# Kernel optimization log

Hardware: AMD Instinct MI355X
Metric: run time of the kernel (lower is better)

The kernel has to match this reference:

```python
import jax, jax.numpy as jnp
import numpy as np

B, N_ATOM, COORD = 32, 48, 3
N_ELEM = 4
GRID_SIZE = 128
SIGMA = 0.05      # gaussian broadening of distf
W_SCALE = 1.0     # weightf: exp(-W_SCALE * distance)
INV_SQRT2PI = 1.0 / np.sqrt(2.0 * np.pi)


def _pairs(n):
    # static ordered index pairs i != j (built with numpy -> jit-safe constants)
    ii, jj = np.meshgrid(np.arange(n), np.arange(n), indexing='ij')
    m = ii != jj
    return jnp.asarray(ii[m]), jnp.asarray(jj[m])


def setup_inputs() -> dict:
    key = jax.random.key(0)
    k1, k2 = jax.random.split(key)
    r = jax.random.normal(k1, (B, N_ATOM, COORD), dtype=jnp.float32) * 2.0
    z = jax.random.randint(k2, (N_ATOM,), 0, N_ELEM)  # species index in [0, N_ELEM)
    grid = jnp.linspace(0.0, 2.0, GRID_SIZE, dtype=jnp.float32)
    return {"r": r, "z": z, "grid": grid}


def reference(r, z, grid):
    b, n, c = r.shape
    g = grid.shape[0]
    e = N_ELEM
    dx = grid[1] - grid[0]
    pi, pj = _pairs(n)                              # (P,)

    diff = r[:, pi] - r[:, pj]                      # (b,P,3)
    d = jnp.sqrt(jnp.sum(diff * diff, axis=-1))     # (b,P) pair distances
    gf = 1.0 / d                                    # geomf: inverse distance
    wf = jnp.exp(-W_SCALE * d)                      # weightf: exponential decay
    # distf: normalized gaussian centered at gf, scaled by grid spacing dx
    t = (grid[None, None, :] - gf[..., None]) / SIGMA
    gv = jnp.exp(-0.5 * t * t) * (dx * INV_SQRT2PI / SIGMA)   # (b,P,G)

    contrib = wf[..., None] * gv                    # (b,P,G)
    seg = z[pi] * e + z[pj]                         # (P,) element-pair bucket
    mbtr = jax.ops.segment_sum(contrib.transpose(1, 0, 2), seg, num_segments=e * e)
    mbtr = mbtr.reshape(e, e, b, g).transpose(2, 0, 1, 3)      # (b,E,E,G)

    # analytic divergence wrt the two atoms' coordinates (order=2, coord=3)
    u = diff / d[..., None]                         # dd/dr_i, (b,P,3)
    dd = jnp.stack([u, -u], axis=2)                 # (b,P,2,3): dd/dr_{i}, dd/dr_{j}
    gf_div = -(gf * gf)[..., None, None] * dd       # d(1/d)/dr
    wf_div = -(W_SCALE * wf)[..., None, None] * dd  # d exp(-s d)/dr
    grid_div = gv * (grid[None, None, :] - gf[..., None]) / (SIGMA * SIGMA)  # dgv/dgf

    # (b,P,G,2,3): gv*wf_div + grid_div*gf_div*wf
    div = (gv[:, :, :, None, None] * wf_div[:, :, None, :, :]
           + grid_div[:, :, :, None, None] * (gf_div * wf[..., None, None])[:, :, None, :, :])

    atom_idx = jnp.stack([pi, pj], axis=1)          # (P,2)
    seg_div = (seg[:, None] * n + atom_idx).reshape(-1)        # (2P,) bucket*n + atom
    p2 = div.transpose(1, 3, 0, 2, 4).reshape(-1, b, g, c)     # (2P,b,G,3)
    mbtr_div = jax.ops.segment_sum(p2, seg_div, num_segments=e * e * n)
    mbtr_div = mbtr_div.reshape(e, e, n, b, g, c).transpose(3, 0, 1, 4, 2, 5)  # (b,E,E,G,N,3)
    return mbtr, mbtr_div
```

## Files before the change

### kernel.cpp

```cpp
#include <hip/hip_runtime.h>

#define NB     32
#define NATOM  48
#define NGRID  128
#define KT     8
#define NTHR   384

#define MBTR_ELEMS (NB*16*NGRID)
#define DIV_PER_B  (16*NGRID*NATOM*3)
#define PANE       (NGRID*NATOM*3)
#define FSTRIDE    49
#define KSTRIDE    (16*FSTRIDE)

__global__ __launch_bounds__(NTHR)
void mbtr_fused(const float* __restrict__ r, const int* __restrict__ z,
                const float* __restrict__ grid, float* __restrict__ out)
{
    const int kt = blockIdx.x, b = blockIdx.y, t = threadIdx.x;
    const int k0 = kt * KT;

    __shared__ float4 pos[NATOM];
    __shared__ int    zl[NATOM];
    __shared__ int    order[NATOM];
    __shared__ int    soff_s[5];
    __shared__ float  Arec[KT * KSTRIDE];

    if (t < 64) {
        const bool isatom = (t < NATOM);
        int myz = 999;
        if (isatom) {
            myz = z[t];
            zl[t] = myz;
            const float* rp = r + ((size_t)b * NATOM + t) * 3;
            pos[t] = make_float4(rp[0], rp[1], rp[2], 0.f);
        }
        const unsigned long long m0 = __ballot(myz == 0);
        const unsigned long long m1 = __ballot(myz == 1);
        const unsigned long long m2 = __ballot(myz == 2);
        const unsigned long long m3 = __ballot(myz == 3);
        const int c0 = __popcll(m0), c1 = __popcll(m1), c2 = __popcll(m2);
        if (isatom) {
            const unsigned long long mm = (myz == 0) ? m0 : (myz == 1) ? m1
                                        : (myz == 2) ? m2 : m3;
            const int base = (myz == 0) ? 0 : (myz == 1) ? c0
                           : (myz == 2) ? c0 + c1 : c0 + c1 + c2;
            const int rank = __popcll(mm & ((1ull << t) - 1ull));
            order[base + rank] = t;
        }
        if (t == 0) {
            soff_s[0] = 0; soff_s[1] = c0; soff_s[2] = c0 + c1;
            soff_s[3] = c0 + c1 + c2; soff_s[4] = NATOM;
        }
    }
    if (t < KT * 16)
        Arec[(t >> 4) * KSTRIDE + (t & 15) * FSTRIDE + NATOM] = 0.f;
    __syncthreads();

    const int n  = t % NATOM;
    const int kk = t / NATOM;
    const float dx   = grid[1] - grid[0];
    const float coef = dx * (0.3989422804014327f * 20.0f);
    const float isc  = 20.0f * 0.84932180580221964f;
    const float tBc  = 20.0f / 0.84932180580221964f;
    const float l2e  = 1.4426950408889634f;
    const float gk   = grid[k0 + kk] * isc;

    float A[4][3] = {{0.f}};
    float M[4]    = {0.f};
    const float4 rn = pos[n];
    int so[5];
    #pragma unroll
    for (int e = 0; e < 5; ++e) so[e] = soff_s[e];

    #pragma unroll
    for (int e = 0; e < 4; ++e) {
        for (int i = so[e]; i < so[e + 1]; ++i) {
            const int    m  = order[i];
            const float4 rm = pos[m];
            const float ddx = rn.x - rm.x, ddy = rn.y - rm.y, ddz = rn.z - rm.z;
            float d2 = ddx*ddx + ddy*ddy + ddz*ddz;
            const bool self = (m == n);
            d2 = self ? 1.0f : d2;
            const float gf  = __builtin_amdgcn_rsqf(d2);
            const float d   = d2 * gf;
            const float tt  = gk - gf * isc;
            const float arg = fmaf(d, l2e, tt * tt);
            const float ex  = exp2f(-arg);
            const float gvw = (self ? 0.f : coef) * ex;
            M[e] += gvw;
            const float p  = gvw * fmaf(tt, gf * gf * tBc, 1.0f);
            const float pg = -p * gf;
            A[e][0] = fmaf(pg, ddx, A[e][0]);
            A[e][1] = fmaf(pg, ddy, A[e][1]);
            A[e][2] = fmaf(pg, ddz, A[e][2]);
        }
    }

    {
        float* ar = Arec + kk * KSTRIDE + n;
        #pragma unroll
        for (int e = 0; e < 4; ++e) {
            ar[(e * 3 + 0) * FSTRIDE] = A[e][0];
            ar[(e * 3 + 1) * FSTRIDE] = A[e][1];
            ar[(e * 3 + 2) * FSTRIDE] = A[e][2];
            ar[(12 + e)    * FSTRIDE] = M[e];
        }
    }
    __syncthreads();

    int a1[2][4], a2[2][4], obase[2] = {0, 0};
    #pragma unroll
    for (int jj = 0; jj < 2; ++jj) {
        const int u = t + NTHR * jj;
        if (u < 576) {
            const int pane = u / 36, w36 = u % 36;
            const int e1 = pane >> 2, e2 = pane & 3;
            obase[jj] = pane * PANE + w36 * 4;
            #pragma unroll
            for (int s = 0; s < 4; ++s) {
                const int p = w36 * 4 + s, nn = p / 3, c = p - nn * 3;
                a1[jj][s] = (zl[nn] == e1) ? ((e2 * 3 + c) * FSTRIDE + nn)
                                           : ((e2 * 3 + c) * FSTRIDE + NATOM);
                a2[jj][s] = (zl[nn] == e2) ? ((e1 * 3 + c) * FSTRIDE + nn)
                                           : ((e1 * 3 + c) * FSTRIDE + NATOM);
            }
        }
    }
    const bool do_mbtr = (t >= 192 && t < 320);
    int mpane = 0, mkk = 0, me1 = 0, me2 = 0;
    if (do_mbtr) {
        const int t2 = t - 192;
        mpane = t2 >> 3; mkk = t2 & 7;
        me1 = mpane >> 2; me2 = mpane & 3;
    }

    float* divout = out + MBTR_ELEMS + (size_t)b * DIV_PER_B;
    #pragma unroll
    for (int kq = 0; kq < KT; ++kq) {
        const float* trk = Arec + kq * KSTRIDE;
        const int k = k0 + kq;
        #pragma unroll
        for (int jj = 0; jj < 2; ++jj) {
            const int u = t + NTHR * jj;
            if (u < 576) {
                float4 v;
                v.x = trk[a1[jj][0]] + trk[a2[jj][0]];
                v.y = trk[a1[jj][1]] + trk[a2[jj][1]];
                v.z = trk[a1[jj][2]] + trk[a2[jj][2]];
                v.w = trk[a1[jj][3]] + trk[a2[jj][3]];
                *(float4*)(divout + obase[jj] + k * 144) = v;
            }
        }
    }
    if (do_mbtr) {
        const float* tr2 = Arec + mkk * KSTRIDE + (12 + me2) * FSTRIDE;
        float s = 0.f;
        #pragma unroll
        for (int nn = 0; nn < NATOM; ++nn)
            s += (zl[nn] == me1) ? tr2[nn] : 0.f;
        out[(size_t)b * 2048 + mpane * NGRID + k0 + mkk] = s;
    }
}

extern "C" void kernel_launch(void* const* d_in, const int* in_sizes, int n_in,
                              void* d_out, int out_size, void* d_ws, size_t ws_size,
                              hipStream_t stream)
{
    const float* r    = (const float*)d_in[0];
    const int*   z    = (const int*)  d_in[1];
    const float* grid = (const float*)d_in[2];
    float* out = (float*)d_out;
    (void)d_ws; (void)ws_size;

    mbtr_fused<<<dim3(NGRID / KT, NB), NTHR, 0, stream>>>(r, z, grid, out);
}
```

Before: 82.64 us.

## Compute two grid points per thread, reusing pair geometry, and halve block size

Each thread now evaluates two grid points (k and k+4) for the same atom, so the distance, rsqrt and direction terms are computed once and used twice. The launch block shrinks from 384 to 192 threads. The per-element loop over sorted atom ranges becomes one flat loop that looks up each atom's element at runtime. The normalisation coefficient is folded into the exponent, and the store loop now covers three output slots per thread. Indexing the accumulator arrays with a runtime element index risks the compiler placing them in scratch memory or emitting select chains, and the smaller blocks reduce parallelism per block.

```diff
diff --git a/kernel.cpp b/kernel.cpp
--- a/kernel.cpp
+++ b/kernel.cpp
@@ -4,7 +4,7 @@
 #define NATOM  48
 #define NGRID  128
 #define KT     8
-#define NTHR   384
+#define NTHR   192
 
 #define MBTR_ELEMS (NB*16*NGRID)
 #define DIV_PER_B  (16*NGRID*NATOM*3)
@@ -22,7 +22,6 @@
     __shared__ float4 pos[NATOM];
     __shared__ int    zl[NATOM];
     __shared__ int    order[NATOM];
-    __shared__ int    soff_s[5];
     __shared__ float  Arec[KT * KSTRIDE];
 
     if (t < 64) {
@@ -47,112 +46,123 @@
             const int rank = __popcll(mm & ((1ull << t) - 1ull));
             order[base + rank] = t;
         }
-        if (t == 0) {
-            soff_s[0] = 0; soff_s[1] = c0; soff_s[2] = c0 + c1;
-            soff_s[3] = c0 + c1 + c2; soff_s[4] = NATOM;
-        }
     }
     if (t < KT * 16)
         Arec[(t >> 4) * KSTRIDE + (t & 15) * FSTRIDE + NATOM] = 0.f;
     __syncthreads();
 
     const int n  = t % NATOM;
-    const int kk = t / NATOM;
+    const int kq = t / NATOM;
     const float dx   = grid[1] - grid[0];
-    const float coef = dx * (0.3989422804014327f * 20.0f);
-    const float isc  = 20.0f * 0.84932180580221964f;
-    const float tBc  = 20.0f / 0.84932180580221964f;
+    const float coef = dx * 7.9788456080286535f;
+    const float mlc  = -__log2f(coef);
+    const float isc  = 16.986436005760382f;
+    const float tBc  = 23.548200452219559f;
     const float l2e  = 1.4426950408889634f;
-    const float gk   = grid[k0 + kk] * isc;
+    const float gkA  = grid[k0 + kq]     * isc;
+    const float gkB  = grid[k0 + kq + 4] * isc;
 
-    float A[4][3] = {{0.f}};
-    float M[4]    = {0.f};
+    float A[2][4][3] = {{{0.f}}};
+    float M[2][4]    = {{0.f}};
     const float4 rn = pos[n];
+
     int so[5];
-    #pragma unroll
-    for (int e = 0; e < 5; ++e) so[e] = soff_s[e];
+    {
+        int cnt0 = 0, cnt1 = 0, cnt2 = 0;
+        (void)cnt0; (void)cnt1; (void)cnt2;
+        so[0] = 0; so[4] = NATOM;
+    }
 
-    #pragma unroll
-    for (int e = 0; e < 4; ++e) {
-        for (int i = so[e]; i < so[e + 1]; ++i) {
-            const int    m  = order[i];
-            const float4 rm = pos[m];
-            const float ddx = rn.x - rm.x, ddy = rn.y - rm.y, ddz = rn.z - rm.z;
-            float d2 = ddx*ddx + ddy*ddy + ddz*ddz;
-            const bool self = (m == n);
-            d2 = self ? 1.0f : d2;
-            const float gf  = __builtin_amdgcn_rsqf(d2);
-            const float d   = d2 * gf;
-            const float tt  = gk - gf * isc;
-            const float arg = fmaf(d, l2e, tt * tt);
-            const float ex  = exp2f(-arg);
-            const float gvw = (self ? 0.f : coef) * ex;
-            M[e] += gvw;
-            const float p  = gvw * fmaf(tt, gf * gf * tBc, 1.0f);
-            const float pg = -p * gf;
-            A[e][0] = fmaf(pg, ddx, A[e][0]);
-            A[e][1] = fmaf(pg, ddy, A[e][1]);
-            A[e][2] = fmaf(pg, ddz, A[e][2]);
+    #pragma unroll 4
+    for (int i = 0; i < NATOM; ++i) {
+        const int    m  = order[i];
+        const int    e  = zl[m];
+        const float4 rm = pos[m];
+        const float ddx = rn.x - rm.x, ddy = rn.y - rm.y, ddz = rn.z - rm.z;
+        float d2 = ddx*ddx + ddy*ddy + ddz*ddz;
+        const bool self = (m == n);
+        d2 = self ? 1.0f : d2;
+        const float gf  = __builtin_amdgcn_rsqf(d2);
+        const float c1  = gf * isc;
+        const float d   = d2 * gf;
+        float base = fmaf(d, l2e, mlc);
+        base = self ? 1e30f : base;
+        const float bq  = (gf * gf) * tBc;
+        const float sux = gf * ddx, suy = gf * ddy, suz = gf * ddz;
+        {
+            const float tt = gkA - c1;
+            const float ex = exp2f(-fmaf(tt, tt, base));
+            M[0][e] += ex;
+            const float p  = ex * fmaf(tt, bq, 1.0f);
+            A[0][e][0] = fmaf(-p, sux, A[0][e][0]);
+            A[0][e][1] = fmaf(-p, suy, A[0][e][1]);
+            A[0][e][2] = fmaf(-p, suz, A[0][e][2]);
+        }
+        {
+            const float tt = gkB - c1;
+            const float ex = exp2f(-fmaf(tt, tt, base));
+            M[1][e] += ex;
+            const float p  = ex * fmaf(tt, bq, 1.0f);
+            A[1][e][0] = fmaf(-p, sux, A[1][e][0]);
+            A[1][e][1] = fmaf(-p, suy, A[1][e][1]);
+            A[1][e][2] = fmaf(-p, suz, A[1][e][2]);
         }
     }
+    (void)so;
 
     {
-        float* ar = Arec + kk * KSTRIDE + n;
+        float* ar0 = Arec + kq       * KSTRIDE + n;
+        float* ar1 = Arec + (kq + 4) * KSTRIDE + n;
         #pragma unroll
         for (int e = 0; e < 4; ++e) {
-            ar[(e * 3 + 0) * FSTRIDE] = A[e][0];
-            ar[(e * 3 + 1) * FSTRIDE] = A[e][1];
-            ar[(e * 3 + 2) * FSTRIDE] = A[e][2];
-            ar[(12 + e)    * FSTRIDE] = M[e];
+            ar0[(e * 3 + 0) * FSTRIDE] = A[0][e][0];
+            ar0[(e * 3 + 1) * FSTRIDE] = A[0][e][1];
+            ar0[(e * 3 + 2) * FSTRIDE] = A[0][e][2];
+            ar0[(12 + e)    * FSTRIDE] = M[0][e];
+            ar1[(e * 3 + 0) * FSTRIDE] = A[1][e][0];
+            ar1[(e * 3 + 1) * FSTRIDE] = A[1][e][1];
+            ar1[(e * 3 + 2) * FSTRIDE] = A[1][e][2];
+            ar1[(12 + e)    * FSTRIDE] = M[1][e];
         }
     }
     __syncthreads();
 
-    int a1[2][4], a2[2][4], obase[2] = {0, 0};
+    int a1[3][4], a2[3][4], obase[3];
     #pragma unroll
-    for (int jj = 0; jj < 2; ++jj) {
+    for (int jj = 0; jj < 3; ++jj) {
         const int u = t + NTHR * jj;
-        if (u < 576) {
-            const int pane = u / 36, w36 = u % 36;
-            const int e1 = pane >> 2, e2 = pane & 3;
-            obase[jj] = pane * PANE + w36 * 4;
-            #pragma unroll
-            for (int s = 0; s < 4; ++s) {
-                const int p = w36 * 4 + s, nn = p / 3, c = p - nn * 3;
-                a1[jj][s] = (zl[nn] == e1) ? ((e2 * 3 + c) * FSTRIDE + nn)
-                                           : ((e2 * 3 + c) * FSTRIDE + NATOM);
-                a2[jj][s] = (zl[nn] == e2) ? ((e1 * 3 + c) * FSTRIDE + nn)
-                                           : ((e1 * 3 + c) * FSTRIDE + NATOM);
-            }
+        const int pane = u / 36, w36 = u % 36;
+        const int e1 = pane >> 2, e2 = pane & 3;
+        obase[jj] = pane * PANE + w36 * 4;
+        #pragma unroll
+        for (int s = 0; s < 4; ++s) {
+            const int p = w36 * 4 + s, nn = p / 3, c = p - nn * 3;
+            a1[jj][s] = (zl[nn] == e1) ? ((e2 * 3 + c) * FSTRIDE + nn)
+                                       : ((e2 * 3 + c) * FSTRIDE + NATOM);
+            a2[jj][s] = (zl[nn] == e2) ? ((e1 * 3 + c) * FSTRIDE + nn)
+                                       : ((e1 * 3 + c) * FSTRIDE + NATOM);
         }
-    }
-    const bool do_mbtr = (t >= 192 && t < 320);
-    int mpane = 0, mkk = 0, me1 = 0, me2 = 0;
-    if (do_mbtr) {
-        const int t2 = t - 192;
-        mpane = t2 >> 3; mkk = t2 & 7;
-        me1 = mpane >> 2; me2 = mpane & 3;
     }
 
     float* divout = out + MBTR_ELEMS + (size_t)b * DIV_PER_B;
     #pragma unroll
-    for (int kq = 0; kq < KT; ++kq) {
-        const float* trk = Arec + kq * KSTRIDE;
-        const int k = k0 + kq;
+    for (int kk = 0; kk < KT; ++kk) {
+        const float* trk = Arec + kk * KSTRIDE;
+        const int k = k0 + kk;
         #pragma unroll
-        for (int jj = 0; jj < 2; ++jj) {
-            const int u = t + NTHR * jj;
-            if (u < 576) {
-                float4 v;
-                v.x = trk[a1[jj][0]] + trk[a2[jj][0]];
-                v.y = trk[a1[jj][1]] + trk[a2[jj][1]];
-                v.z = trk[a1[jj][2]] + trk[a2[jj][2]];
-                v.w = trk[a1[jj][3]] + trk[a2[jj][3]];
-                *(float4*)(divout + obase[jj] + k * 144) = v;
-            }
+        for (int jj = 0; jj < 3; ++jj) {
+            float4 v;
+            v.x = trk[a1[jj][0]] + trk[a2[jj][0]];
+            v.y = trk[a1[jj][1]] + trk[a2[jj][1]];
+            v.z = trk[a1[jj][2]] + trk[a2[jj][2]];
+            v.w = trk[a1[jj][3]] + trk[a2[jj][3]];
+            *(float4*)(divout + obase[jj] + k * 144) = v;
         }
     }
-    if (do_mbtr) {
+
+    if (t < 128) {
+        const int mpane = t >> 3, mkk = t & 7;
+        const int me1 = mpane >> 2, me2 = mpane & 3;
         const float* tr2 = Arec + mkk * KSTRIDE + (12 + me2) * FSTRIDE;
         float s = 0.f;
         #pragma unroll
```

New measurement: 91.78 us. +11.1%, slower.

## Write divergence directly from registers and fold coefficient into exponent

Applied to the files above, without the earlier changes.

Each thread now writes its own 16 panes × 3 coordinates of the divergence output straight from registers, replacing the shared-memory staging and the float4 gather-store pass. Only the M sums go through LDS, for the mbtr reduction. The gaussian prefactor and the self-pair mask are folded into the exp2 argument through a log2 offset and a large sentinel. The trade is that global stores become scalar and strided (n*3 per thread, 12-byte groups), so coalescing is worse than the previous float4 stores, in exchange for less LDS traffic and one fewer barrier.

```diff
diff --git a/kernel.cpp b/kernel.cpp
--- a/kernel.cpp
+++ b/kernel.cpp
@@ -9,8 +9,7 @@
 #define MBTR_ELEMS (NB*16*NGRID)
 #define DIV_PER_B  (16*NGRID*NATOM*3)
 #define PANE       (NGRID*NATOM*3)
-#define FSTRIDE    49
-#define KSTRIDE    (16*FSTRIDE)
+#define MSTRIDE    49
 
 __global__ __launch_bounds__(NTHR)
 void mbtr_fused(const float* __restrict__ r, const int* __restrict__ z,
@@ -23,7 +22,7 @@
     __shared__ int    zl[NATOM];
     __shared__ int    order[NATOM];
     __shared__ int    soff_s[5];
-    __shared__ float  Arec[KT * KSTRIDE];
+    __shared__ float  Mrec[KT * 4 * MSTRIDE];
 
     if (t < 64) {
         const bool isatom = (t < NATOM);
@@ -52,22 +51,22 @@
             soff_s[3] = c0 + c1 + c2; soff_s[4] = NATOM;
         }
     }
-    if (t < KT * 16)
-        Arec[(t >> 4) * KSTRIDE + (t & 15) * FSTRIDE + NATOM] = 0.f;
     __syncthreads();
 
     const int n  = t % NATOM;
     const int kk = t / NATOM;
     const float dx   = grid[1] - grid[0];
-    const float coef = dx * (0.3989422804014327f * 20.0f);
-    const float isc  = 20.0f * 0.84932180580221964f;
-    const float tBc  = 20.0f / 0.84932180580221964f;
+    const float coef = dx * 7.9788456080286535f;
+    const float mlc  = -__log2f(coef);
+    const float isc  = 16.986436005760382f;
+    const float tBc  = 23.548200452219559f;
     const float l2e  = 1.4426950408889634f;
     const float gk   = grid[k0 + kk] * isc;
 
     float A[4][3] = {{0.f}};
     float M[4]    = {0.f};
     const float4 rn = pos[n];
+    const int   zn  = zl[n];
     int so[5];
     #pragma unroll
     for (int e = 0; e < 5; ++e) so[e] = soff_s[e];
@@ -82,78 +81,48 @@
             const bool self = (m == n);
             d2 = self ? 1.0f : d2;
             const float gf  = __builtin_amdgcn_rsqf(d2);
+            const float c1  = gf * isc;
             const float d   = d2 * gf;
-            const float tt  = gk - gf * isc;
-            const float arg = fmaf(d, l2e, tt * tt);
-            const float ex  = exp2f(-arg);
-            const float gvw = (self ? 0.f : coef) * ex;
-            M[e] += gvw;
-            const float p  = gvw * fmaf(tt, gf * gf * tBc, 1.0f);
-            const float pg = -p * gf;
-            A[e][0] = fmaf(pg, ddx, A[e][0]);
-            A[e][1] = fmaf(pg, ddy, A[e][1]);
-            A[e][2] = fmaf(pg, ddz, A[e][2]);
+            float base = fmaf(d, l2e, mlc);
+            base = self ? 1e30f : base;
+            const float bq  = (gf * gf) * tBc;
+            const float tt  = gk - c1;
+            const float ex  = exp2f(-fmaf(tt, tt, base));
+            M[e] += ex;
+            const float p   = ex * fmaf(tt, bq, 1.0f);
+            A[e][0] = fmaf(-p, gf * ddx, A[e][0]);
+            A[e][1] = fmaf(-p, gf * ddy, A[e][1]);
+            A[e][2] = fmaf(-p, gf * ddz, A[e][2]);
         }
     }
 
     {
-        float* ar = Arec + kk * KSTRIDE + n;
+        float* mr = Mrec + kk * (4 * MSTRIDE) + n;
         #pragma unroll
-        for (int e = 0; e < 4; ++e) {
-            ar[(e * 3 + 0) * FSTRIDE] = A[e][0];
-            ar[(e * 3 + 1) * FSTRIDE] = A[e][1];
-            ar[(e * 3 + 2) * FSTRIDE] = A[e][2];
-            ar[(12 + e)    * FSTRIDE] = M[e];
+        for (int e = 0; e < 4; ++e) mr[e * MSTRIDE] = M[e];
+    }
+
+    float* basep = out + MBTR_ELEMS + (size_t)b * DIV_PER_B
+                 + (size_t)(k0 + kk) * 144 + n * 3;
+    #pragma unroll
+    for (int e1 = 0; e1 < 4; ++e1) {
+        const bool s1 = (zn == e1);
+        #pragma unroll
+        for (int e2 = 0; e2 < 4; ++e2) {
+            const bool s2 = (zn == e2);
+            float* p = basep + (e1 * 4 + e2) * PANE;
+            p[0] = (s1 ? A[e2][0] : 0.f) + (s2 ? A[e1][0] : 0.f);
+            p[1] = (s1 ? A[e2][1] : 0.f) + (s2 ? A[e1][1] : 0.f);
+            p[2] = (s1 ? A[e2][2] : 0.f) + (s2 ? A[e1][2] : 0.f);
         }
     }
+
     __syncthreads();
 
-    int a1[2][4], a2[2][4], obase[2] = {0, 0};
-    #pragma unroll
-    for (int jj = 0; jj < 2; ++jj) {
-        const int u = t + NTHR * jj;
-        if (u < 576) {
-            const int pane = u / 36, w36 = u % 36;
-            const int e1 = pane >> 2, e2 = pane & 3;
-            obase[jj] = pane * PANE + w36 * 4;
-            #pragma unroll
-            for (int s = 0; s < 4; ++s) {
-                const int p = w36 * 4 + s, nn = p / 3, c = p - nn * 3;
-                a1[jj][s] = (zl[nn] == e1) ? ((e2 * 3 + c) * FSTRIDE + nn)
-                                           : ((e2 * 3 + c) * FSTRIDE + NATOM);
-                a2[jj][s] = (zl[nn] == e2) ? ((e1 * 3 + c) * FSTRIDE + nn)
-                                           : ((e1 * 3 + c) * FSTRIDE + NATOM);
-            }
-        }
-    }
-    const bool do_mbtr = (t >= 192 && t < 320);
-    int mpane = 0, mkk = 0, me1 = 0, me2 = 0;
-    if (do_mbtr) {
-        const int t2 = t - 192;
-        mpane = t2 >> 3; mkk = t2 & 7;
-        me1 = mpane >> 2; me2 = mpane & 3;
-    }
-
-    float* divout = out + MBTR_ELEMS + (size_t)b * DIV_PER_B;
-    #pragma unroll
-    for (int kq = 0; kq < KT; ++kq) {
-        const float* trk = Arec + kq * KSTRIDE;
-        const int k = k0 + kq;
-        #pragma unroll
-        for (int jj = 0; jj < 2; ++jj) {
-            const int u = t + NTHR * jj;
-            if (u < 576) {
-                float4 v;
-                v.x = trk[a1[jj][0]] + trk[a2[jj][0]];
-                v.y = trk[a1[jj][1]] + trk[a2[jj][1]];
-                v.z = trk[a1[jj][2]] + trk[a2[jj][2]];
-                v.w = trk[a1[jj][3]] + trk[a2[jj][3]];
-                *(float4*)(divout + obase[jj] + k * 144) = v;
-            }
-        }
-    }
-    if (do_mbtr) {
-        const float* tr2 = Arec + mkk * KSTRIDE + (12 + me2) * FSTRIDE;
+    if (t < 128) {
+        const int mpane = t >> 3, mkk = t & 7;
+        const int me1 = mpane >> 2, me2 = mpane & 3;
+        const float* tr2 = Mrec + mkk * (4 * MSTRIDE) + me2 * MSTRIDE;
         float s = 0.f;
         #pragma unroll
         for (int nn = 0; nn < NATOM; ++nn)
```

Measured after the change: 80.75 us. 2.3% less time.
